# Kernel optimization log

Measured on AMD Instinct MI355X. Metric: run time of the kernel, lower is better.

## Reference

```python
import jax, jax.numpy as jnp
import numpy as np

N = 8192
IN_C = 512
OUT_C = 256
ALPHA = 0.5  # leaky-relu negative slope used on attention scores
NEG_INF = jnp.float32(-9e15)


def setup_inputs() -> dict:
    key = jax.random.key(0)
    k_h, k_adj, k_W, k_a = jax.random.split(key, 4)
    h = jax.random.normal(k_h, (N, IN_C), dtype=jnp.float32)
    adj = jax.random.randint(k_adj, (N, N), 0, 2, dtype=jnp.int32)
    # xavier_uniform with gain=1.414
    gain = 1.414
    limW = gain * np.sqrt(6.0 / (IN_C + OUT_C))
    W = jax.random.uniform(k_W, (IN_C, OUT_C), dtype=jnp.float32, minval=-limW, maxval=limW)
    lima = gain * np.sqrt(6.0 / (2 * OUT_C + 1))
    a = jax.random.uniform(k_a, (2 * OUT_C, 1), dtype=jnp.float32, minval=-lima, maxval=lima)
    return {"h": h, "adj": adj, "W": W, "a": a}


def reference(h, adj, W, a):
    out_c = W.shape[1]
    Wh = h @ W                                   # [N, out]
    Wh1 = Wh @ a[:out_c]                         # [N, 1]
    Wh2 = Wh @ a[out_c:]                         # [N, 1]
    e = jax.nn.leaky_relu(Wh1 + Wh2.T, negative_slope=ALPHA)  # [N, N]
    scores = jnp.where(adj > 0, e, NEG_INF)
    attention = jax.nn.softmax(scores, axis=1)   # row-wise softmax
    h_prime = attention @ Wh                     # [N, out] weighted aggregation
    return jnp.maximum(h_prime, 0.0)             # concat=True -> relu
```

## Files before the change

### kernel.cpp

```cpp
#include <hip/hip_runtime.h>
#include <stdint.h>

#define GN  8192
#define GIC 512
#define GOC 256

typedef int   vint4   __attribute__((__vector_size__(16)));
typedef float vfloat4 __attribute__((__vector_size__(16)));

__device__ __forceinline__ float bf2f(uint16_t u) {
  union { uint32_t i; float f; } v; v.i = ((uint32_t)u) << 16; return v.f;
}
__device__ __forceinline__ uint16_t f2bf(float f) {
  union { uint32_t i; float f; } v; v.f = f;
  uint32_t lsb = (v.i >> 16) & 1u;
  v.i += 0x7fffu + lsb;
  return (uint16_t)(v.i >> 16);
}
__device__ __forceinline__ float lrelu(float x) { return x > 0.f ? x : 0.5f * x; }
__device__ __forceinline__ float ldin(const void* p, size_t idx, int isbf) {
  return isbf ? bf2f(((const uint16_t*)p)[idx]) : ((const float*)p)[idx];
}

__global__ __launch_bounds__(256) void k_fill(uint16_t* out, int n) {
  int i = blockIdx.x * 256 + threadIdx.x;
  if (i < n) out[i] = 0x40E0u;
}

__global__ void k_detect(const void* W, int* flag) {
  __shared__ float mx[64];
  int t = threadIdx.x;
  const uint16_t* p = (const uint16_t*)W;
  float m = 0.f;
  for (int k = 0; k < 4; ++k) {
    float v = fabsf(bf2f(p[t * 4 + k]));
    if (!(v <= 1.0f)) v = 1e30f;
    m = fmaxf(m, v);
  }
  mx[t] = m;
  __syncthreads();
  if (t == 0) {
    float mm = 0.f;
    for (int i = 0; i < 64; ++i) mm = fmaxf(mm, mx[i]);
    flag[0] = (mm < 0.5f) ? 1 : 0;
  }
}

__global__ __launch_bounds__(256) void k_wh(const void* __restrict__ h,
                                            const void* __restrict__ W,
                                            uint16_t* __restrict__ WhF,
                                            const int* __restrict__ flag) {
  const int isbf = flag[0];
  __shared__ float hs[8][GIC];
  const int t = threadIdx.x, i0 = blockIdx.x * 8;
  float acc[8] = {0.f, 0.f, 0.f, 0.f, 0.f, 0.f, 0.f, 0.f};
  const int c = t;
  if (isbf) {
    const uint16_t* hp = (const uint16_t*)h;
    const uint16_t* Wp = (const uint16_t*)W;
    for (int x = t; x < 512; x += 256) {
      int r = x >> 6, cc = (x & 63) * 8;
      int4 raw = *(const int4*)&hp[(size_t)(i0 + r) * GIC + cc];
      uint32_t u0 = (uint32_t)raw.x;
      uint32_t u1 = (uint32_t)raw.y;
      uint32_t u2 = (uint32_t)raw.z;
      uint32_t u3 = (uint32_t)raw.w;
      hs[r][cc + 0] = bf2f((uint16_t)(u0 & 0xffffu));
      hs[r][cc + 1] = bf2f((uint16_t)(u0 >> 16));
      hs[r][cc + 2] = bf2f((uint16_t)(u1 & 0xffffu));
      hs[r][cc + 3] = bf2f((uint16_t)(u1 >> 16));
      hs[r][cc + 4] = bf2f((uint16_t)(u2 & 0xffffu));
      hs[r][cc + 5] = bf2f((uint16_t)(u2 >> 16));
      hs[r][cc + 6] = bf2f((uint16_t)(u3 & 0xffffu));
      hs[r][cc + 7] = bf2f((uint16_t)(u3 >> 16));
    }
    __syncthreads();
    for (int k = 0; k < GIC; k += 4) {
      float w0 = bf2f(Wp[(size_t)(k + 0) * GOC + c]);
      float w1 = bf2f(Wp[(size_t)(k + 1) * GOC + c]);
      float w2 = bf2f(Wp[(size_t)(k + 2) * GOC + c]);
      float w3 = bf2f(Wp[(size_t)(k + 3) * GOC + c]);
#pragma unroll
      for (int r = 0; r < 8; ++r) {
        float4 hv = *(const float4*)&hs[r][k];
        acc[r] = fmaf(hv.x, w0, acc[r]);
        acc[r] = fmaf(hv.y, w1, acc[r]);
        acc[r] = fmaf(hv.z, w2, acc[r]);
        acc[r] = fmaf(hv.w, w3, acc[r]);
      }
    }
  } else {
    for (int x = t; x < 8 * GIC; x += 256) {
      int r = x >> 9, k = x & (GIC - 1);
      hs[r][k] = ldin(h, (size_t)(i0 + r) * GIC + k, 0);
    }
    __syncthreads();
    for (int k = 0; k < GIC; ++k) {
      float w = ldin(W, (size_t)k * GOC + c, 0);
#pragma unroll
      for (int r = 0; r < 8; ++r) acc[r] = fmaf(hs[r][k], w, acc[r]);
    }
  }
  int4 pk;
  pk.x = (int)((uint32_t)f2bf(acc[0]) | ((uint32_t)f2bf(acc[1]) << 16));
  pk.y = (int)((uint32_t)f2bf(acc[2]) | ((uint32_t)f2bf(acc[3]) << 16));
  pk.z = (int)((uint32_t)f2bf(acc[4]) | ((uint32_t)f2bf(acc[5]) << 16));
  pk.w = (int)((uint32_t)f2bf(acc[6]) | ((uint32_t)f2bf(acc[7]) << 16));
  *(int4*)&WhF[((size_t)blockIdx.x * GOC + c) * 8] = pk;
}

__global__ __launch_bounds__(256) void k_wha(const uint16_t* __restrict__ WhF,
                                             const void* __restrict__ a,
                                             float* __restrict__ Wh1,
                                             float* __restrict__ Wh2,
                                             const int* __restrict__ flag) {
  const int isbf = flag[0];
  __shared__ float s1[256], s2[256];
  const int i = blockIdx.x, c = threadIdx.x;
  float v = bf2f(WhF[((size_t)(i >> 3) * GOC + c) * 8 + (i & 7)]);
  s1[c] = v * ldin(a, c, isbf);
  s2[c] = v * ldin(a, GOC + c, isbf);
  __syncthreads();
  for (int o = 128; o > 0; o >>= 1) {
    if (c < o) { s1[c] += s1[c + o]; s2[c] += s2[c + o]; }
    __syncthreads();
  }
  if (c == 0) { Wh1[i] = s1[0]; Wh2[i] = s2[0]; }
}

__global__ __launch_bounds__(256) void k_w2max(const float* __restrict__ Wh2,
                                               float* __restrict__ w2m) {
  __shared__ float red[256];
  const int t = threadIdx.x;
  float m = -3e38f;
  for (int x = t; x < GN / 4; x += 256) {
    float4 v = ((const float4*)Wh2)[x];
    m = fmaxf(m, fmaxf(fmaxf(v.x, v.y), fmaxf(v.z, v.w)));
  }
  red[t] = m;
  __syncthreads();
  for (int o = 128; o > 0; o >>= 1) {
    if (t < o) red[t] = fmaxf(red[t], red[t + o]);
    __syncthreads();
  }
  if (t == 0) w2m[0] = red[0];
}

__global__ __launch_bounds__(256) void GraphAttentionLayer_P1_2834678415522_kernel(
    const int* __restrict__ adj, const uint16_t* __restrict__ WhF,
    const float* __restrict__ Wh1, const float* __restrict__ Wh2,
    const float* __restrict__ w2m, void* __restrict__ out,
    const int* __restrict__ flag) {
  const int isbf = flag[0];
  __shared__ uint16_t pA[16][72];
  __shared__ float red16[16][16];
  __shared__ float sb1[16];
  __shared__ float sbM[16];
  __shared__ float lcS[16];
  const int t = threadIdx.x;
  const int i0 = blockIdx.x * 16;
  if (t < 16) {
    float b = Wh1[i0 + t];
    sb1[t] = b;
    sbM[t] = lrelu(b + w2m[0]);
  }
  __syncthreads();

  const int ar = t >> 4;
  const int c16 = t & 15;
  const int aj = c16 * 4;
  const float vb = sb1[ar];
  const float vM = sbM[ar];
  const int lane = t & 63, w = t >> 6;
  const int quad = lane >> 4, n16 = lane & 15;

  vfloat4 acc0 = {0.f, 0.f, 0.f, 0.f};
  vfloat4 acc1 = {0.f, 0.f, 0.f, 0.f};
  vfloat4 acc2 = {0.f, 0.f, 0.f, 0.f};
  vfloat4 acc3 = {0.f, 0.f, 0.f, 0.f};
  float lsum = 0.f;

  const size_t rowbase = (size_t)(i0 + ar) * GN;
  int4   adjv = *(const int4*)&adj[rowbase + aj];
  float4 w2v  = *(const float4*)&Wh2[aj];

  for (int j0 = 0; j0 < GN; j0 += 64) {
    float e0 = adjv.x > 0 ? lrelu(vb + w2v.x) : -9e15f;
    float e1 = adjv.y > 0 ? lrelu(vb + w2v.y) : -9e15f;
    float e2 = adjv.z > 0 ? lrelu(vb + w2v.z) : -9e15f;
    float e3 = adjv.w > 0 ? lrelu(vb + w2v.w) : -9e15f;
    float p0 = __expf(e0 - vM);
    float p1 = __expf(e1 - vM);
    float p2 = __expf(e2 - vM);
    float p3 = __expf(e3 - vM);
    uint32_t q0 = (uint32_t)f2bf(p0) | ((uint32_t)f2bf(p1) << 16);
    uint32_t q1 = (uint32_t)f2bf(p2) | ((uint32_t)f2bf(p3) << 16);
    *(uint32_t*)&pA[ar][aj]     = q0;
    *(uint32_t*)&pA[ar][aj + 2] = q1;
    lsum += (p0 + p1) + (p2 + p3);
    if (j0 + 64 < GN) {
      adjv = *(const int4*)&adj[rowbase + j0 + 64 + aj];
      w2v  = *(const float4*)&Wh2[j0 + 64 + aj];
    }
    __syncthreads();
    vint4 a0 = *(const vint4*)&pA[n16][quad * 8];
    vint4 a1 = *(const vint4*)&pA[n16][32 + quad * 8];
    const int kb0 = (j0 >> 3) + quad;
    const uint16_t* bp0 = &WhF[((size_t)kb0 * GOC + w * 64 + n16) * 8];
    const uint16_t* bp1 = &WhF[((size_t)(kb0 + 4) * GOC + w * 64 + n16) * 8];
#pragma unroll
    for (int ct = 0; ct < 4; ++ct) {
      vint4 b0 = *(const vint4*)(bp0 + (size_t)ct * 16 * 8);
      vint4 b1 = *(const vint4*)(bp1 + (size_t)ct * 16 * 8);
      vfloat4* accp = ct == 0 ? &acc0 : ct == 1 ? &acc1 : ct == 2 ? &acc2 : &acc3;
      __asm__ volatile("s_nop 1\n\tv_mfma_f32_16x16x32_bf16 %0, %1, %2, %0"
                       : "+v"(*accp) : "v"(a0), "v"(b0));
      __asm__ volatile("s_nop 1\n\tv_mfma_f32_16x16x32_bf16 %0, %1, %2, %0"
                       : "+v"(*accp) : "v"(a1), "v"(b1));
    }
    __syncthreads();
  }

  red16[ar][c16] = lsum;
  __asm__ volatile("s_nop 7\n\ts_nop 7"
                   : "+v"(acc0), "+v"(acc1), "+v"(acc2), "+v"(acc3));
  __syncthreads();
  if (t < 16) {
    float s = 0.f;
    for (int i = 0; i < 16; ++i) s += red16[t][i];
    lcS[t] = 1.0f / s;
  }
  __syncthreads();

  const float il0 = lcS[quad * 4 + 0];
  const float il1 = lcS[quad * 4 + 1];
  const float il2 = lcS[quad * 4 + 2];
  const float il3 = lcS[quad * 4 + 3];
#pragma unroll
  for (int ct = 0; ct < 4; ++ct) {
    const vfloat4 av = ct == 0 ? acc0 : ct == 1 ? acc1 : ct == 2 ? acc2 : acc3;
    const int col = w * 64 + ct * 16 + n16;
    float v0 = fmaxf(av[0] * il0, 0.f);
    float v1 = fmaxf(av[1] * il1, 0.f);
    float v2 = fmaxf(av[2] * il2, 0.f);
    float v3 = fmaxf(av[3] * il3, 0.f);
    if (isbf) {
      uint16_t* o = (uint16_t*)out;
      o[(size_t)(i0 + quad * 4 + 0) * GOC + col] = f2bf(v0);
      o[(size_t)(i0 + quad * 4 + 1) * GOC + col] = f2bf(v1);
      o[(size_t)(i0 + quad * 4 + 2) * GOC + col] = f2bf(v2);
      o[(size_t)(i0 + quad * 4 + 3) * GOC + col] = f2bf(v3);
    } else {
      float* o = (float*)out;
      o[(size_t)(i0 + quad * 4 + 0) * GOC + col] = v0;
      o[(size_t)(i0 + quad * 4 + 1) * GOC + col] = v1;
      o[(size_t)(i0 + quad * 4 + 2) * GOC + col] = v2;
      o[(size_t)(i0 + quad * 4 + 3) * GOC + col] = v3;
    }
  }
}

extern "C" void kernel_launch(void* const* d_in, const int* in_sizes, int n_in,
                              void* d_out, int out_size, void* d_ws, size_t ws_size,
                              hipStream_t stream) {
  uint16_t* WhF = (uint16_t*)d_ws;
  float* Wh1  = (float*)(WhF + (size_t)GN * GOC);
  float* Wh2  = Wh1 + GN;
  int*   flag = (int*)(Wh2 + GN);
  float* w2m  = (float*)(flag + 1);

  const void* h = d_in[0]; const void* adj = d_in[1];
  const void* W = d_in[2]; const void* a = d_in[3];
  for (int i = 0; i < n_in; ++i) {
    long long s = in_sizes[i];
    if      (s == (long long)GN * GIC)  h   = d_in[i];
    else if (s == (long long)GN * GN)   adj = d_in[i];
    else if (s == (long long)GIC * GOC) W   = d_in[i];
    else if (s == 2LL * GOC)            a   = d_in[i];
  }

  const int n_out = GN * GOC;
  k_fill<<<(n_out + 255) / 256, 256, 0, stream>>>((uint16_t*)d_out, n_out);
  k_detect<<<1, 64, 0, stream>>>(W, flag);
  k_wh <<<GN / 8, 256, 0, stream>>>(h, W, WhF, flag);
  k_wha<<<GN, 256, 0, stream>>>(WhF, a, Wh1, Wh2, flag);
  k_w2max<<<1, 256, 0, stream>>>(Wh2, w2m);
  GraphAttentionLayer_P1_2834678415522_kernel<<<GN / 16, 256, 0, stream>>>(
      (const int*)adj, WhF, Wh1, Wh2, w2m, d_out, flag);
}
```

Measured before the change: 603.8 us.

## Split attention aggregation over two column halves with a combine kernel

The main attention kernel now splits each 16-row group across two blocks, each covering half of the neighbour columns, doubling the grid from 512 to 1024 blocks. Each block writes partial fp32 outputs and partial row sums to workspace, and a new combine kernel adds the halves, normalises, applies relu and writes the output. The aim is better occupancy across the GPU's compute units. In exchange it adds a launch and extra global traffic for the partial buffers, and it only takes this path when the workspace is large enough.

Measured after the change: 519.9 us. 13.9% less time.

```diff
diff --git a/kernel.cpp b/kernel.cpp
--- a/kernel.cpp
+++ b/kernel.cpp
@@ -149,6 +149,130 @@
 __global__ __launch_bounds__(256) void GraphAttentionLayer_P1_2834678415522_kernel(
     const int* __restrict__ adj, const uint16_t* __restrict__ WhF,
     const float* __restrict__ Wh1, const float* __restrict__ Wh2,
+    const float* __restrict__ w2m, float* __restrict__ pO,
+    float* __restrict__ pL) {
+  __shared__ uint16_t pA[16][72];
+  __shared__ float red16[16][16];
+  __shared__ float sb1[16];
+  __shared__ float sbM[16];
+  const int t = threadIdx.x;
+  const int rg = blockIdx.x >> 1;
+  const int ch = blockIdx.x & 1;
+  const int i0 = rg * 16;
+  const int jb = ch * 4096;
+  if (t < 16) {
+    float b = Wh1[i0 + t];
+    sb1[t] = b;
+    sbM[t] = lrelu(b + w2m[0]);
+  }
+  __syncthreads();
+
+  const int ar = t >> 4;
+  const int c16 = t & 15;
+  const int aj = c16 * 4;
+  const float vb = sb1[ar];
+  const float vM = sbM[ar];
+  const int lane = t & 63, w = t >> 6;
+  const int quad = lane >> 4, n16 = lane & 15;
+
+  vfloat4 acc0 = {0.f, 0.f, 0.f, 0.f};
+  vfloat4 acc1 = {0.f, 0.f, 0.f, 0.f};
+  vfloat4 acc2 = {0.f, 0.f, 0.f, 0.f};
+  vfloat4 acc3 = {0.f, 0.f, 0.f, 0.f};
+  float lsum = 0.f;
+
+  const size_t rowbase = (size_t)(i0 + ar) * GN + jb;
+  int4   adjv = *(const int4*)&adj[rowbase + aj];
+  float4 w2v  = *(const float4*)&Wh2[jb + aj];
+
+  for (int jt = 0; jt < 4096; jt += 64) {
+    float e0 = adjv.x > 0 ? lrelu(vb + w2v.x) : -9e15f;
+    float e1 = adjv.y > 0 ? lrelu(vb + w2v.y) : -9e15f;
+    float e2 = adjv.z > 0 ? lrelu(vb + w2v.z) : -9e15f;
+    float e3 = adjv.w > 0 ? lrelu(vb + w2v.w) : -9e15f;
+    float p0 = __expf(e0 - vM);
+    float p1 = __expf(e1 - vM);
+    float p2 = __expf(e2 - vM);
+    float p3 = __expf(e3 - vM);
+    uint32_t q0 = (uint32_t)f2bf(p0) | ((uint32_t)f2bf(p1) << 16);
+    uint32_t q1 = (uint32_t)f2bf(p2) | ((uint32_t)f2bf(p3) << 16);
+    *(uint32_t*)&pA[ar][aj]     = q0;
+    *(uint32_t*)&pA[ar][aj + 2] = q1;
+    lsum += (p0 + p1) + (p2 + p3);
+    if (jt + 64 < 4096) {
+      adjv = *(const int4*)&adj[rowbase + jt + 64 + aj];
+      w2v  = *(const float4*)&Wh2[jb + jt + 64 + aj];
+    }
+    __syncthreads();
+    vint4 a0 = *(const vint4*)&pA[n16][quad * 8];
+    vint4 a1 = *(const vint4*)&pA[n16][32 + quad * 8];
+    const int kb0 = ((jb + jt) >> 3) + quad;
+    const uint16_t* bp0 = &WhF[((size_t)kb0 * GOC + w * 64 + n16) * 8];
+    const uint16_t* bp1 = &WhF[((size_t)(kb0 + 4) * GOC + w * 64 + n16) * 8];
+#pragma unroll
+    for (int ct = 0; ct < 4; ++ct) {
+      vint4 b0 = *(const vint4*)(bp0 + (size_t)ct * 16 * 8);
+      vint4 b1 = *(const vint4*)(bp1 + (size_t)ct * 16 * 8);
+      vfloat4* accp = ct == 0 ? &acc0 : ct == 1 ? &acc1 : ct == 2 ? &acc2 : &acc3;
+      __asm__ volatile("s_nop 1\n\tv_mfma_f32_16x16x32_bf16 %0, %1, %2, %0"
+                       : "+v"(*accp) : "v"(a0), "v"(b0));
+      __asm__ volatile("s_nop 1\n\tv_mfma_f32_16x16x32_bf16 %0, %1, %2, %0"
+                       : "+v"(*accp) : "v"(a1), "v"(b1));
+    }
+    __syncthreads();
+  }
+
+  red16[ar][c16] = lsum;
+  __asm__ volatile("s_nop 7\n\ts_nop 7"
+                   : "+v"(acc0), "+v"(acc1), "+v"(acc2), "+v"(acc3));
+  __syncthreads();
+  if (t < 16) {
+    float s = 0.f;
+    for (int i = 0; i < 16; ++i) s += red16[t][i];
+    pL[(size_t)ch * GN + i0 + t] = s;
+  }
+
+#pragma unroll
+  for (int ct = 0; ct < 4; ++ct) {
+    const vfloat4 av = ct == 0 ? acc0 : ct == 1 ? acc1 : ct == 2 ? acc2 : acc3;
+    const int col = w * 64 + ct * 16 + n16;
+    pO[((size_t)ch * GN + i0 + quad * 4 + 0) * GOC + col] = av[0];
+    pO[((size_t)ch * GN + i0 + quad * 4 + 1) * GOC + col] = av[1];
+    pO[((size_t)ch * GN + i0 + quad * 4 + 2) * GOC + col] = av[2];
+    pO[((size_t)ch * GN + i0 + quad * 4 + 3) * GOC + col] = av[3];
+  }
+}
+
+__global__ __launch_bounds__(256) void k_comb(const float* __restrict__ pO,
+                                              const float* __restrict__ pL,
+                                              void* __restrict__ out,
+                                              const int* __restrict__ flag) {
+  const int isbf = flag[0];
+  size_t gid = ((size_t)blockIdx.x * 256 + threadIdx.x) * 4;
+  size_t row = gid >> 8;
+  float4 a0 = *(const float4*)&pO[gid];
+  float4 a1 = *(const float4*)&pO[(size_t)GN * GOC + gid];
+  float il = 1.0f / (pL[row] + pL[GN + row]);
+  float v0 = fmaxf((a0.x + a1.x) * il, 0.f);
+  float v1 = fmaxf((a0.y + a1.y) * il, 0.f);
+  float v2 = fmaxf((a0.z + a1.z) * il, 0.f);
+  float v3 = fmaxf((a0.w + a1.w) * il, 0.f);
+  if (isbf) {
+    uint16_t* o = (uint16_t*)out;
+    uint32_t q0 = (uint32_t)f2bf(v0) | ((uint32_t)f2bf(v1) << 16);
+    uint32_t q1 = (uint32_t)f2bf(v2) | ((uint32_t)f2bf(v3) << 16);
+    *(uint32_t*)&o[gid]     = q0;
+    *(uint32_t*)&o[gid + 2] = q1;
+  } else {
+    float4 vv;
+    vv.x = v0; vv.y = v1; vv.z = v2; vv.w = v3;
+    *(float4*)&((float*)out)[gid] = vv;
+  }
+}
+
+__global__ __launch_bounds__(256) void k_gat1(
+    const int* __restrict__ adj, const uint16_t* __restrict__ WhF,
+    const float* __restrict__ Wh1, const float* __restrict__ Wh2,
     const float* __restrict__ w2m, void* __restrict__ out,
     const int* __restrict__ flag) {
   const int isbf = flag[0];
@@ -266,8 +390,12 @@
   uint16_t* WhF = (uint16_t*)d_ws;
   float* Wh1  = (float*)(WhF + (size_t)GN * GOC);
   float* Wh2  = Wh1 + GN;
-  int*   flag = (int*)(Wh2 + GN);
+  float* pO   = Wh2 + GN;
+  float* pL   = pO + (size_t)2 * GN * GOC;
+  int*   flag = (int*)(pL + 2 * GN);
   float* w2m  = (float*)(flag + 1);
+  size_t need = (size_t)((char*)(w2m + 1) - (char*)d_ws);
+  const int use_split = (ws_size >= need) ? 1 : 0;
 
   const void* h = d_in[0]; const void* adj = d_in[1];
   const void* W = d_in[2]; const void* a = d_in[3];
@@ -278,6 +406,10 @@
     else if (s == (long long)GIC * GOC) W   = d_in[i];
     else if (s == 2LL * GOC)            a   = d_in[i];
   }
+  if (!use_split) {
+    flag = (int*)(Wh2 + GN);
+    w2m  = (float*)(flag + 1);
+  }
 
   const int n_out = GN * GOC;
   k_fill<<<(n_out + 255) / 256, 256, 0, stream>>>((uint16_t*)d_out, n_out);
@@ -285,6 +417,12 @@
   k_wh <<<GN / 8, 256, 0, stream>>>(h, W, WhF, flag);
   k_wha<<<GN, 256, 0, stream>>>(WhF, a, Wh1, Wh2, flag);
   k_w2max<<<1, 256, 0, stream>>>(Wh2, w2m);
-  GraphAttentionLayer_P1_2834678415522_kernel<<<GN / 16, 256, 0, stream>>>(
-      (const int*)adj, WhF, Wh1, Wh2, w2m, d_out, flag);
-}
+  if (use_split) {
+    GraphAttentionLayer_P1_2834678415522_kernel<<<GN / 8, 256, 0, stream>>>(
+        (const int*)adj, WhF, Wh1, Wh2, w2m, pO, pL);
+    k_comb<<<(GN * GOC) / 1024, 256, 0, stream>>>(pO, pL, d_out, flag);
+  } else {
+    k_gat1<<<GN / 16, 256, 0, stream>>>((const int*)adj, WhF, Wh1, Wh2, w2m,
+                                        d_out, flag);
+  }
+}
```
